# Kernel tuning notes

Measured on AMD Instinct MI355X. Metric: run time of the kernel, lower is better.

The kernel has to match this reference:

```python
import jax, jax.numpy as jnp
import numpy as np

SIZE = 128  # matches init_kwargs output_shape
EPS = 1e-12  # numerical floor for 1 - sum_of_squares (original TF code has none; values stay >0 analytically)


def _chol_from_z(zvec):
    """Build lower-triangular Cholesky factor of a correlation matrix from
    canonical partial-correlation parameters z (|z|<1), per batch row.
    Column j: zeros above, diag = sqrt(1 - s[j]), below-diag = z[i,j]*sqrt(1 - s[i]),
    where s accumulates the row-wise sum of squares of previous columns.
    """
    B = zvec.shape[0]
    n = SIZE
    rows, cols = np.tril_indices(n, -1)  # strictly lower triangle, row-major (matches l_indices)
    z = jnp.zeros((B, n, n), zvec.dtype).at[:, rows, cols].set(zvec)  # [B,n,n]
    i = jnp.arange(n)

    def step(s, xs):
        zcol, j = xs                      # zcol: [B,n] = z[:, :, j]
        sq = jnp.sqrt(jnp.clip(1.0 - s, EPS))  # [B,n] = sqrt(1 - running sum of squares)
        col = jnp.where(i == j, sq, jnp.where(i > j, zcol * sq, 0.0))
        return s + col * col, col

    s0 = jnp.zeros((B, n), zvec.dtype)
    _, cols_out = jax.lax.scan(step, s0, (jnp.moveaxis(z, 2, 0), i))  # cols_out: [n(col), B, n(row)]
    return jnp.transpose(cols_out, (1, 2, 0))  # [B, n, n], L[b, row, col]


def setup_inputs() -> dict:
    key = jax.random.key(0)
    B = 2048
    nz = SIZE * (SIZE - 1) // 2  # 8128
    # canonical partial correlations must lie in (-1, 1)
    zvec = jax.random.uniform(key, (B, nz), jnp.float32, -0.9, 0.9)
    return {"inputs": zvec}


def reference(inputs):
    return _chol_from_z(inputs)
```

## Files before the change

kernel.cpp:

```cpp
#include <hip/hip_runtime.h>

#define NROW 128
#define NZ   8128
#define EPSF 1e-12f

#define DPP_MUL(x, ctrl, rmask)                                               \
  x *= __int_as_float(__builtin_amdgcn_update_dpp(                            \
      0x3f800000, __float_as_int(x), ctrl, rmask, 0xF, false))

__global__ __launch_bounds__(256) void chol_from_z_kernel(
    const float* __restrict__ z, float* __restrict__ out)
{
    const int gtid = blockIdx.x * blockDim.x + threadIdx.x;
    const int w    = gtid >> 6;
    const int lane = threadIdx.x & 63;
    const int half = lane >> 5;
    const int l    = lane & 31;

    const int row = (w << 1) | half;
    const int b   = row >> 7;
    const int i   = row & 127;

    const float* __restrict__ zr = z + (size_t)b * NZ + (size_t)((i * (i - 1)) >> 1);
    const int base = l << 2;

    float zt[4];
    #pragma unroll
    for (int t = 0; t < 4; ++t) {
        const int p = base + t;
        zt[t] = (p < i) ? zr[p] : 0.0f;
    }

    float c0 = fmaf(-zt[0], zt[0], 1.0f);
    float c1 = c0 * fmaf(-zt[1], zt[1], 1.0f);
    float c2 = c1 * fmaf(-zt[2], zt[2], 1.0f);
    float c3 = c2 * fmaf(-zt[3], zt[3], 1.0f);

    float x = c3;
    DPP_MUL(x, 0x111, 0xF);
    DPP_MUL(x, 0x112, 0xF);
    DPP_MUL(x, 0x114, 0xF);
    DPP_MUL(x, 0x118, 0xF);
    DPP_MUL(x, 0x142, 0xA);

    const float e = x * __builtin_amdgcn_rcpf(c3);

    const float pre0 = e;
    const float pre1 = e * c0;
    const float pre2 = e * c1;
    const float pre3 = e * c2;

    const float sq0 = __builtin_amdgcn_sqrtf(fmaxf(pre0, EPSF));
    const float sq1 = __builtin_amdgcn_sqrtf(fmaxf(pre1, EPSF));
    const float sq2 = __builtin_amdgcn_sqrtf(fmaxf(pre2, EPSF));
    const float sq3 = __builtin_amdgcn_sqrtf(fmaxf(pre3, EPSF));

    const float o0 = (base + 0 == i) ? sq0 : zt[0] * sq0;
    const float o1 = (base + 1 == i) ? sq1 : zt[1] * sq1;
    const float o2 = (base + 2 == i) ? sq2 : zt[2] * sq2;
    const float o3 = (base + 3 == i) ? sq3 : zt[3] * sq3;

    *reinterpret_cast<float4*>(out + (size_t)row * NROW + base) =
        make_float4(o0, o1, o2, o3);
}

extern "C" void kernel_launch(void* const* d_in, const int* in_sizes, int n_in,
                              void* d_out, int out_size, void* d_ws, size_t ws_size,
                              hipStream_t stream)
{
    const float* z = (const float*)d_in[0];
    float* out = (float*)d_out;

    const int B = in_sizes[0] / NZ;
    const int nrows_total = B * NROW;
    const int nwaves = nrows_total >> 1;

    const int block = 256;
    const int grid = (nwaves * 64) / block;
    chol_from_z_kernel<<<grid, block, 0, stream>>>(z, out);
}
```

Before: 39.75 us.

## Interleave row elements across lanes with strided loads and per-chunk DPP scans

Switches each lane from owning four contiguous elements to owning four elements strided by 32, so each of the four loads and stores becomes fully coalesced across the half-wave. The row-wise prefix product of (1 - z^2) is now done with four independent DPP scans combined through ds_swizzle broadcasts of the chunk totals. This replaces float4 stores and per-lane scalar loads with scalar coalesced accesses, at the cost of four times the DPP work plus extra swizzle and reciprocal instructions.

```diff
diff --git a/kernel.cpp b/kernel.cpp
--- a/kernel.cpp
+++ b/kernel.cpp
@@ -22,46 +22,57 @@
     const int i   = row & 127;
 
     const float* __restrict__ zr = z + (size_t)b * NZ + (size_t)((i * (i - 1)) >> 1);
-    const int base = l << 2;
 
-    float zt[4];
+    float zq[4], f[4], r[4];
     #pragma unroll
-    for (int t = 0; t < 4; ++t) {
-        const int p = base + t;
-        zt[t] = (p < i) ? zr[p] : 0.0f;
+    for (int q = 0; q < 4; ++q) {
+        const int p = (q << 5) + l;
+        zq[q] = (p < i) ? zr[p] : 0.0f;
+        f[q]  = fmaf(-zq[q], zq[q], 1.0f);
+        r[q]  = __builtin_amdgcn_rcpf(f[q]);
     }
 
-    float c0 = fmaf(-zt[0], zt[0], 1.0f);
-    float c1 = c0 * fmaf(-zt[1], zt[1], 1.0f);
-    float c2 = c1 * fmaf(-zt[2], zt[2], 1.0f);
-    float c3 = c2 * fmaf(-zt[3], zt[3], 1.0f);
+    float g[4];
+    #pragma unroll
+    for (int q = 0; q < 4; ++q) {
+        float x = f[q];
+        DPP_MUL(x, 0x111, 0xF);
+        DPP_MUL(x, 0x112, 0xF);
+        DPP_MUL(x, 0x114, 0xF);
+        DPP_MUL(x, 0x118, 0xF);
+        DPP_MUL(x, 0x142, 0xA);
+        g[q] = x;
+    }
 
-    float x = c3;
-    DPP_MUL(x, 0x111, 0xF);
-    DPP_MUL(x, 0x112, 0xF);
-    DPP_MUL(x, 0x114, 0xF);
-    DPP_MUL(x, 0x118, 0xF);
-    DPP_MUL(x, 0x142, 0xA);
+    const float t0 = __int_as_float(__builtin_amdgcn_ds_swizzle(__float_as_int(g[0]), 0x3E0));
+    const float t1 = __int_as_float(__builtin_amdgcn_ds_swizzle(__float_as_int(g[1]), 0x3E0));
+    const float t2 = __int_as_float(__builtin_amdgcn_ds_swizzle(__float_as_int(g[2]), 0x3E0));
 
-    const float e = x * __builtin_amdgcn_rcpf(c3);
+    const float R1 = t0;
+    const float R2 = t0 * t1;
+    const float R3 = R2 * t2;
 
-    const float pre0 = e;
-    const float pre1 = e * c0;
-    const float pre2 = e * c1;
-    const float pre3 = e * c2;
+    const float pre0 =      g[0] * r[0];
+    const float pre1 = R1 * (g[1] * r[1]);
+    const float pre2 = R2 * (g[2] * r[2]);
+    const float pre3 = R3 * (g[3] * r[3]);
 
     const float sq0 = __builtin_amdgcn_sqrtf(fmaxf(pre0, EPSF));
     const float sq1 = __builtin_amdgcn_sqrtf(fmaxf(pre1, EPSF));
     const float sq2 = __builtin_amdgcn_sqrtf(fmaxf(pre2, EPSF));
     const float sq3 = __builtin_amdgcn_sqrtf(fmaxf(pre3, EPSF));
 
-    const float o0 = (base + 0 == i) ? sq0 : zt[0] * sq0;
-    const float o1 = (base + 1 == i) ? sq1 : zt[1] * sq1;
-    const float o2 = (base + 2 == i) ? sq2 : zt[2] * sq2;
-    const float o3 = (base + 3 == i) ? sq3 : zt[3] * sq3;
+    const int p0 = l, p1 = 32 + l, p2 = 64 + l, p3 = 96 + l;
+    const float o0 = (p0 == i) ? sq0 : zq[0] * sq0;
+    const float o1 = (p1 == i) ? sq1 : zq[1] * sq1;
+    const float o2 = (p2 == i) ? sq2 : zq[2] * sq2;
+    const float o3 = (p3 == i) ? sq3 : zq[3] * sq3;
 
-    *reinterpret_cast<float4*>(out + (size_t)row * NROW + base) =
-        make_float4(o0, o1, o2, o3);
+    float* __restrict__ orow = out + (size_t)row * NROW + l;
+    orow[0]  = o0;
+    orow[32] = o1;
+    orow[64] = o2;
+    orow[96] = o3;
 }
 
 extern "C" void kernel_launch(void* const* d_in, const int* in_sizes, int n_in,
```

New measurement: 38.00 us. -4.4%, faster.
